# Performance work log

Hardware: AMD Instinct MI355X
Metric: run time of the kernel (lower is better)

The kernel has to match this reference:

```python
import jax, jax.numpy as jnp
import numpy as np

N, N_SPINS, N_HIDDEN = 8192, 1024, 1024


def setup_inputs() -> dict:
    key = jax.random.key(0)
    ks = jax.random.split(key, 6)
    s_in = 1.0 / np.sqrt(N_SPINS)
    s_h = 1.0 / np.sqrt(N_HIDDEN)
    return {
        "x": jax.random.normal(ks[0], (N, N_SPINS), dtype=jnp.float32),
        "W_in": jax.random.normal(ks[1], (N_HIDDEN, N_SPINS), dtype=jnp.float32) * s_in,
        "b_in": jax.random.normal(ks[2], (N_HIDDEN,), dtype=jnp.float32) * s_in,
        "Wq": jax.random.normal(ks[3], (N_HIDDEN, N_HIDDEN), dtype=jnp.float32) * s_h,
        "Wk": jax.random.normal(ks[4], (N_HIDDEN, N_HIDDEN), dtype=jnp.float32) * s_h,
        "Wv": jax.random.normal(ks[5], (N_HIDDEN, N_HIDDEN), dtype=jnp.float32) * s_h,
    }


def reference(x, W_in, b_in, Wq, Wk, Wv):
    # embedding: Linear(n_spins, n_hidden)  -> h: [N, H]
    h = x @ W_in.T + b_in
    q = h @ Wq.T                      # [N, H]
    k = h @ Wk.T                      # [N, H]
    v = h @ Wv.T                      # [N, H]
    scores = (q @ k.T) * 0.25         # [N, N], scale 1/4 as in source
    attn = jax.nn.softmax(scores, axis=0)  # softmax over dim=0 (columns)
    out = attn @ v                    # [N, H]
    # log(cosh(z)) = |z| + log1p(exp(-2|z|)) - log(2), numerically stable
    a = jnp.abs(out)
    logcosh = a + jnp.log1p(jnp.exp(-2.0 * a)) - jnp.log(jnp.asarray(2.0, out.dtype))
    return jnp.sum(logcosh, axis=-1)  # [N]
```

## Files before the change

### kernel.cpp

```cpp
#include <hip/hip_runtime.h>
#include <hip/hip_bf16.h>
#include <cstdint>
#include <cstddef>

#define NTOK 8192
#define NHID 1024

typedef __attribute__((ext_vector_type(8))) __bf16 bf16x8;
typedef __attribute__((ext_vector_type(4))) float f32x4;

__device__ __forceinline__ unsigned short f2bf(float f) {
    union { float f; unsigned u; } v; v.f = f;
    unsigned r = v.u + 0x7FFF + ((v.u >> 16) & 1);
    return (unsigned short)(r >> 16);
}

__device__ __forceinline__ float bf2f(unsigned short u) {
    union { unsigned u; float f; } v; v.u = ((unsigned)u) << 16;
    return v.f;
}

__device__ __forceinline__ void async_copy16(const void* gsrc, void* ldsdst) {
    __builtin_amdgcn_global_load_lds(
        (const __attribute__((address_space(1))) unsigned int*)gsrc,
        (__attribute__((address_space(3))) unsigned int*)ldsdst,
        16, 0, 0);
}

__device__ __forceinline__ void read_frags(
    const unsigned short* __restrict__ As, const unsigned short* __restrict__ Bs,
    int wm, int wn, int fr, int pc, bf16x8 (&a)[8], bf16x8 (&b)[4])
{
#pragma unroll
    for (int i = 0; i < 8; ++i) a[i] = *(const bf16x8*)&As[(wm + i * 16 + fr) * 64 + pc];
#pragma unroll
    for (int j = 0; j < 4; ++j) b[j] = *(const bf16x8*)&Bs[(wn + j * 16 + fr) * 64 + pc];
}

__device__ __forceinline__ void mfma32(
    const bf16x8 (&a)[8], const bf16x8 (&b)[4], f32x4 (&acc)[8][4])
{
    __builtin_amdgcn_s_setprio(1);
#pragma unroll
    for (int i = 0; i < 8; ++i)
#pragma unroll
        for (int j = 0; j < 4; ++j)
            acc[i][j] = __builtin_amdgcn_mfma_f32_16x16x32_bf16(
                a[i], b[j], acc[i][j], 0, 0, 0);
    __builtin_amdgcn_s_setprio(0);
}

template <int EPI, bool SWAP>
__global__ __launch_bounds__(512, 2) void gemm_sq2(
    const unsigned short* __restrict__ A,
    const unsigned short* __restrict__ B,
    void* __restrict__ C,
    const float* __restrict__ bias,
    float* __restrict__ zsum,
    float scale, int M, int N, int K, int lda, int ldb)
{
    __shared__ __attribute__((aligned(16))) unsigned short lds[2][32768];

    const int tid  = threadIdx.x;
    const int wave = tid >> 6;
    const int lane = tid & 63;
    const int bm = (SWAP ? blockIdx.x : blockIdx.y) * 256;
    const int bn = (SWAP ? blockIdx.y : blockIdx.x) * 256;
    const size_t ldaz = (size_t)lda;
    const size_t ldbz = (size_t)ldb;

    const int srow = lane >> 3;
    const int scol = ((lane & 7) ^ srow) * 8;
    const unsigned short* Ag[4];
    const unsigned short* Bg[4];
    int off[4];
#pragma unroll
    for (int t = 0; t < 4; ++t) {
        int r = (wave * 4 + t) * 8 + srow;
        Ag[t] = A + (size_t)(bm + r) * ldaz + scol;
        Bg[t] = B + (size_t)(bn + r) * ldbz + scol;
        off[t] = (wave * 4 + t) * 512;
    }

    const int wm = (wave >> 2) * 128;
    const int wn = (wave & 3) * 64;
    const int fr = lane & 15;
    const int frl = fr & 7;
    const int q = lane >> 4;

    const int pc0 = (q ^ frl) * 8;
    const int pc1 = ((4 + q) ^ frl) * 8;

    f32x4 acc[8][4] = {};

    const int nt = K >> 6;

    auto stageA = [&](int s) {
#pragma unroll
        for (int t = 0; t < 4; ++t) { async_copy16(Ag[t], &lds[s][off[t]]); Ag[t] += 64; }
    };
    auto stageB = [&](int s) {
#pragma unroll
        for (int t = 0; t < 4; ++t) { async_copy16(Bg[t], &lds[s][16384 + off[t]]); Bg[t] += 64; }
    };

    stageA(0);
    stageB(0);
    stageA(1);
    asm volatile("s_waitcnt vmcnt(4)" ::: "memory");
    asm volatile("s_barrier" ::: "memory");

    bf16x8 aP[8], bP[4];
    bf16x8 aQ[8], bQ[4];
    read_frags(&lds[0][0], &lds[0][16384], wm, wn, fr, pc0, aP, bP);

    for (int t = 0; t < nt; ++t) {
        const int cb = t & 1;
        const int nb = cb ^ 1;
        const unsigned short* As = &lds[cb][0];
        const unsigned short* Bs = &lds[cb][16384];

        if (t + 1 < nt) stageB(nb);
        read_frags(As, Bs, wm, wn, fr, pc1, aQ, bQ);
        __builtin_amdgcn_sched_barrier(0);
        mfma32(aP, bP, acc);
        asm volatile("s_waitcnt lgkmcnt(0)" ::: "memory");
        asm volatile("s_barrier" ::: "memory");
        if (t + 2 < nt) stageA(cb);
        if (t < nt - 2) asm volatile("s_waitcnt vmcnt(4)" ::: "memory");
        else            asm volatile("s_waitcnt vmcnt(0)" ::: "memory");
        asm volatile("s_barrier" ::: "memory");

        if (t + 1 < nt)
            read_frags(&lds[nb][0], &lds[nb][16384], wm, wn, fr, pc0, aP, bP);
        __builtin_amdgcn_sched_barrier(0);
        mfma32(aQ, bQ, acc);
    }

    const int erow = q * 4;
#pragma unroll
    for (int j = 0; j < 4; ++j) {
        const int gcol = bn + wn + j * 16 + fr;
        const float bv = (EPI == 1 && bias) ? bias[gcol] : 0.0f;
        float colsum = 0.0f;
#pragma unroll
        for (int i = 0; i < 8; ++i) {
            const int grow0 = bm + wm + i * 16 + erow;
#pragma unroll
            for (int r = 0; r < 4; ++r) {
                float v;
                if (EPI == 2) {
                    v = __expf(fmaf(acc[i][j][r], scale, -64.0f));
                    colsum += v;
                } else {
                    v = acc[i][j][r] * scale + bv;
                }
                size_t idx = (size_t)(grow0 + r) * N + gcol;
                if (EPI == 0) ((float*)C)[idx] = v;
                else          ((unsigned short*)C)[idx] = f2bf(v);
            }
        }
        if (EPI == 2) {
            colsum += __shfl_xor(colsum, 16, 64);
            colsum += __shfl_xor(colsum, 32, 64);
            if (q == 0) atomicAdd(&zsum[gcol], colsum);
        }
    }
}

template <int EPI, bool SWAP>
__global__ __launch_bounds__(512, 2) void gemm_bt4(
    const unsigned short* __restrict__ A,
    const unsigned short* __restrict__ B,
    void* __restrict__ C,
    const float* __restrict__ bias,
    float* __restrict__ zsum,
    float scale, int M, int N, int K, int lda, int ldb)
{
    __shared__ __attribute__((aligned(16))) unsigned short lds[3][24576];

    const int tid  = threadIdx.x;
    const int wave = tid >> 6;
    const int lane = tid & 63;
    const int bm = (SWAP ? blockIdx.x : blockIdx.y) * 256;
    const int bn = (SWAP ? blockIdx.y : blockIdx.x) * 128;
    const size_t ldaz = (size_t)lda;
    const size_t ldbz = (size_t)ldb;

    const int srow = lane >> 3;
    const int scol = ((lane & 7) ^ srow) * 8;
    const unsigned short* Ag[4];
    const unsigned short* Bg[2];
    int Aoff[4], Boff[2];
#pragma unroll
    for (int t = 0; t < 4; ++t) {
        int r = (wave * 4 + t) * 8 + srow;
        Ag[t] = A + (size_t)(bm + r) * ldaz + scol;
        Aoff[t] = (wave * 4 + t) * 512;
    }
#pragma unroll
    for (int t = 0; t < 2; ++t) {
        int r = (wave * 2 + t) * 8 + srow;
        Bg[t] = B + (size_t)(bn + r) * ldbz + scol;
        Boff[t] = 16384 + (wave * 2 + t) * 512;
    }

    const int wm = (wave >> 1) * 64;
    const int wn = (wave & 1) * 64;
    const int fr = lane & 15;
    const int frl = fr & 7;
    const int q = lane >> 4;

    const int pc0 = (q ^ frl) * 8;
    const int pc1 = ((4 + q) ^ frl) * 8;

    f32x4 acc[4][4] = {};

    const int nt = K >> 6;

    {
        unsigned short* b0 = &lds[0][0];
        unsigned short* b1 = &lds[1][0];
#pragma unroll
        for (int u = 0; u < 4; ++u) { async_copy16(Ag[u], b0 + Aoff[u]); Ag[u] += 64; }
#pragma unroll
        for (int u = 0; u < 2; ++u) { async_copy16(Bg[u], b0 + Boff[u]); Bg[u] += 64; }
#pragma unroll
        for (int u = 0; u < 4; ++u) { async_copy16(Ag[u], b1 + Aoff[u]); Ag[u] += 64; }
#pragma unroll
        for (int u = 0; u < 2; ++u) { async_copy16(Bg[u], b1 + Boff[u]); Bg[u] += 64; }
        asm volatile("s_waitcnt vmcnt(6)" ::: "memory");
        asm volatile("s_barrier" ::: "memory");
    }

    bf16x8 a0_0, a0_1, a0_2, a0_3, b0_0, b0_1, b0_2, b0_3;
    bf16x8 a1_0, a1_1, a1_2, a1_3, b1_0, b1_1, b1_2, b1_3;

    {
        const unsigned short* As = &lds[0][0];
        const unsigned short* Bs = &lds[0][16384];
        a0_0 = *(const bf16x8*)&As[(wm +  0 + fr) * 64 + pc0];
        a0_1 = *(const bf16x8*)&As[(wm + 16 + fr) * 64 + pc0];
        a0_2 = *(const bf16x8*)&As[(wm + 32 + fr) * 64 + pc0];
        a0_3 = *(const bf16x8*)&As[(wm + 48 + fr) * 64 + pc0];
        b0_0 = *(const bf16x8*)&Bs[(wn +  0 + fr) * 64 + pc0];
        b0_1 = *(const bf16x8*)&Bs[(wn + 16 + fr) * 64 + pc0];
        b0_2 = *(const bf16x8*)&Bs[(wn + 32 + fr) * 64 + pc0];
        b0_3 = *(const bf16x8*)&Bs[(wn + 48 + fr) * 64 + pc0];
    }

#define MFMA16(AA0, AA1, AA2, AA3, BB0, BB1, BB2, BB3)                         \
    do {                                                                       \
        __builtin_amdgcn_s_setprio(1);                                         \
        acc[0][0] = __builtin_amdgcn_mfma_f32_16x16x32_bf16(AA0, BB0, acc[0][0], 0, 0, 0); \
        acc[0][1] = __builtin_amdgcn_mfma_f32_16x16x32_bf16(AA0, BB1, acc[0][1], 0, 0, 0); \
        acc[0][2] = __builtin_amdgcn_mfma_f32_16x16x32_bf16(AA0, BB2, acc[0][2], 0, 0, 0); \
        acc[0][3] = __builtin_amdgcn_mfma_f32_16x16x32_bf16(AA0, BB3, acc[0][3], 0, 0, 0); \
        acc[1][0] = __builtin_amdgcn_mfma_f32_16x16x32_bf16(AA1, BB0, acc[1][0], 0, 0, 0); \
        acc[1][1] = __builtin_amdgcn_mfma_f32_16x16x32_bf16(AA1, BB1, acc[1][1], 0, 0, 0); \
        acc[1][2] = __builtin_amdgcn_mfma_f32_16x16x32_bf16(AA1, BB2, acc[1][2], 0, 0, 0); \
        acc[1][3] = __builtin_amdgcn_mfma_f32_16x16x32_bf16(AA1, BB3, acc[1][3], 0, 0, 0); \
        acc[2][0] = __builtin_amdgcn_mfma_f32_16x16x32_bf16(AA2, BB0, acc[2][0], 0, 0, 0); \
        acc[2][1] = __builtin_amdgcn_mfma_f32_16x16x32_bf16(AA2, BB1, acc[2][1], 0, 0, 0); \
        acc[2][2] = __builtin_amdgcn_mfma_f32_16x16x32_bf16(AA2, BB2, acc[2][2], 0, 0, 0); \
        acc[2][3] = __builtin_amdgcn_mfma_f32_16x16x32_bf16(AA2, BB3, acc[2][3], 0, 0, 0); \
        acc[3][0] = __builtin_amdgcn_mfma_f32_16x16x32_bf16(AA3, BB0, acc[3][0], 0, 0, 0); \
        acc[3][1] = __builtin_amdgcn_mfma_f32_16x16x32_bf16(AA3, BB1, acc[3][1], 0, 0, 0); \
        acc[3][2] = __builtin_amdgcn_mfma_f32_16x16x32_bf16(AA3, BB2, acc[3][2], 0, 0, 0); \
        acc[3][3] = __builtin_amdgcn_mfma_f32_16x16x32_bf16(AA3, BB3, acc[3][3], 0, 0, 0); \
        __builtin_amdgcn_s_setprio(0);                                         \
    } while (0)

    int cb = 0;
    int sb = 2;
    for (int t = 0; t < nt; ++t) {
        const bool pf = (t + 2 < nt);
        const unsigned short* As = &lds[cb][0];
        const unsigned short* Bs = &lds[cb][16384];
        unsigned short* Sb = &lds[sb][0];
        const int nb = (cb == 2) ? 0 : cb + 1;
        const unsigned short* An = &lds[nb][0];
        const unsigned short* Bn = &lds[nb][16384];

        a1_0 = *(const bf16x8*)&As[(wm +  0 + fr) * 64 + pc1];
        a1_1 = *(const bf16x8*)&As[(wm + 16 + fr) * 64 + pc1];
        a1_2 = *(const bf16x8*)&As[(wm + 32 + fr) * 64 + pc1];
        a1_3 = *(const bf16x8*)&As[(wm + 48 + fr) * 64 + pc1];
        b1_0 = *(const bf16x8*)&Bs[(wn +  0 + fr) * 64 + pc1];
        b1_1 = *(const bf16x8*)&Bs[(wn + 16 + fr) * 64 + pc1];
        b1_2 = *(const bf16x8*)&Bs[(wn + 32 + fr) * 64 + pc1];
        b1_3 = *(const bf16x8*)&Bs[(wn + 48 + fr) * 64 + pc1];
        if (pf) {
#pragma unroll
            for (int u = 0; u < 4; ++u) { async_copy16(Ag[u], Sb + Aoff[u]); Ag[u] += 64; }
        }
        __builtin_amdgcn_sched_barrier(0);
        MFMA16(a0_0, a0_1, a0_2, a0_3, b0_0, b0_1, b0_2, b0_3);
        if (t < nt - 2) asm volatile("s_waitcnt vmcnt(4)" ::: "memory");
        else            asm volatile("s_waitcnt vmcnt(0)" ::: "memory");
        asm volatile("s_barrier" ::: "memory");

        if (t + 1 < nt) {
            a0_0 = *(const bf16x8*)&An[(wm +  0 + fr) * 64 + pc0];
            a0_1 = *(const bf16x8*)&An[(wm + 16 + fr) * 64 + pc0];
            a0_2 = *(const bf16x8*)&An[(wm + 32 + fr) * 64 + pc0];
            a0_3 = *(const bf16x8*)&An[(wm + 48 + fr) * 64 + pc0];
            b0_0 = *(const bf16x8*)&Bn[(wn +  0 + fr) * 64 + pc0];
            b0_1 = *(const bf16x8*)&Bn[(wn + 16 + fr) * 64 + pc0];
            b0_2 = *(const bf16x8*)&Bn[(wn + 32 + fr) * 64 + pc0];
            b0_3 = *(const bf16x8*)&Bn[(wn + 48 + fr) * 64 + pc0];
        }
        if (pf) {
#pragma unroll
            for (int u = 0; u < 2; ++u) { async_copy16(Bg[u], Sb + Boff[u]); Bg[u] += 64; }
        }
        __builtin_amdgcn_sched_barrier(0);
        MFMA16(a1_0, a1_1, a1_2, a1_3, b1_0, b1_1, b1_2, b1_3);
        asm volatile("s_barrier" ::: "memory");

        if (pf) sb = (sb == 2) ? 0 : sb + 1;
        cb = nb;
    }
#undef MFMA16

    const int erow = q * 4;
#pragma unroll
    for (int j = 0; j < 4; ++j) {
        const int gcol = bn + wn + j * 16 + fr;
        const float bv = (EPI == 1 && bias) ? bias[gcol] : 0.0f;
        float colsum = 0.0f;
#pragma unroll
        for (int i = 0; i < 4; ++i) {
            const int grow0 = bm + wm + i * 16 + erow;
#pragma unroll
            for (int r = 0; r < 4; ++r) {
                float v;
                if (EPI == 2) {
                    v = __expf(fmaf(acc[i][j][r], scale, -64.0f));
                    colsum += v;
                } else {
                    v = acc[i][j][r] * scale + bv;
                }
                size_t idx = (size_t)(grow0 + r) * N + gcol;
                if (EPI == 0) ((float*)C)[idx] = v;
                else          ((unsigned short*)C)[idx] = f2bf(v);
            }
        }
        if (EPI == 2) {
            colsum += __shfl_xor(colsum, 16, 64);
            colsum += __shfl_xor(colsum, 32, 64);
            if (q == 0) atomicAdd(&zsum[gcol], colsum);
        }
    }
}

__global__ void cvt_all(const float4* __restrict__ x,
                        const float4* __restrict__ w0,
                        const float4* __restrict__ w1,
                        const float4* __restrict__ w2,
                        const float4* __restrict__ w3,
                        ushort4* __restrict__ xb,
                        ushort4* __restrict__ wdst,
                        float4* __restrict__ pz4,
                        int n4x, int n4w)
{
    int i = blockIdx.x * blockDim.x + threadIdx.x;
    int n4 = n4x + 4 * n4w;
    if (i >= n4) {
        int zi = i - n4;
        if (zi < 2048) pz4[zi] = make_float4(0.f, 0.f, 0.f, 0.f);
        return;
    }
    float4 f;
    ushort4* dst;
    if (i < n4x) {
        f = x[i]; dst = xb + i;
    } else {
        int r = i - n4x;
        int seg = r / n4w, off = r % n4w;
        const float4* src = (seg == 0) ? w0 : (seg == 1) ? w1 : (seg == 2) ? w2 : w3;
        f = src[off]; dst = wdst + r;
    }
    ushort4 o;
    o.x = f2bf(f.x); o.y = f2bf(f.y); o.z = f2bf(f.z); o.w = f2bf(f.w);
    *dst = o;
}

__global__ __launch_bounds__(256) void transpose_scale(
    const unsigned short* __restrict__ v,
    const float* __restrict__ z,
    unsigned short* __restrict__ vt)
{
    __shared__ float lds[64 * 65];
    const int tid = threadIdx.x;
    const int j0 = blockIdx.x * 64;
    const int h0 = blockIdx.y * 64;
    const int c = tid & 63;
    const int r0 = tid >> 6;
#pragma unroll
    for (int it = 0; it < 16; ++it) {
        int r = it * 4 + r0;
        lds[r * 65 + c] = bf2f(v[(size_t)(j0 + r) * 3072 + h0 + c]);
    }
    __syncthreads();
    const float rz = 1.0f / z[j0 + c];
#pragma unroll
    for (int it = 0; it < 16; ++it) {
        int r = it * 4 + r0;
        vt[(size_t)(h0 + r) * NTOK + j0 + c] = f2bf(lds[c * 65 + r] * rz);
    }
}

__global__ void logcosh_rowsum(const ushort4* __restrict__ O4,
                               float* __restrict__ out)
{
    const float LN2 = 0.69314718055994531f;
    int row = blockIdx.x;
    ushort4 u = O4[(size_t)row * 256 + threadIdx.x];
    float s = 0.0f, a;
    a = fabsf(bf2f(u.x)); s += a + log1pf(__expf(-2.0f * a));
    a = fabsf(bf2f(u.y)); s += a + log1pf(__expf(-2.0f * a));
    a = fabsf(bf2f(u.z)); s += a + log1pf(__expf(-2.0f * a));
    a = fabsf(bf2f(u.w)); s += a + log1pf(__expf(-2.0f * a));
    s -= 4.0f * LN2;
    for (int off = 32; off; off >>= 1) s += __shfl_down(s, off, 64);
    __shared__ float red[4];
    if ((threadIdx.x & 63) == 0) red[threadIdx.x >> 6] = s;
    __syncthreads();
    if (threadIdx.x == 0) out[row] = red[0] + red[1] + red[2] + red[3];
}

extern "C" void kernel_launch(void* const* d_in, const int* in_sizes, int n_in,
                              void* d_out, int out_size, void* d_ws, size_t ws_size,
                              hipStream_t stream)
{
    (void)in_sizes; (void)n_in; (void)out_size; (void)ws_size;

    const float* x    = (const float*)d_in[0];
    const float* W_in = (const float*)d_in[1];
    const float* b_in = (const float*)d_in[2];
    const float* Wq   = (const float*)d_in[3];
    const float* Wk   = (const float*)d_in[4];
    const float* Wv   = (const float*)d_in[5];
    float* out = (float*)d_out;

    char* w = (char*)d_ws;
    const size_t MiB = 1024 * 1024;
    unsigned short* Pb     = (unsigned short*)(w);
    unsigned short* qkv    = (unsigned short*)(w + 128 * MiB);
    unsigned short* xb     = (unsigned short*)(w + 128 * MiB);
    unsigned short* outb   = (unsigned short*)(w + 128 * MiB);
    unsigned short* hb     = (unsigned short*)(w + 176 * MiB);
    unsigned short* vtb    = (unsigned short*)(w + 176 * MiB);
    unsigned short* wib    = (unsigned short*)(w + 192 * MiB);
    unsigned short* wqkvb  = (unsigned short*)(w + 194 * MiB);
    float*          pz     = (float*)         (w + 200 * MiB);

    {
        int n4x = NTOK * NHID / 4;
        int n4w = NHID * NHID / 4;
        int n4  = n4x + 4 * n4w;
        cvt_all<<<n4 / 256 + 8, 256, 0, stream>>>(
            (const float4*)x, (const float4*)W_in, (const float4*)Wq,
            (const float4*)Wk, (const float4*)Wv,
            (ushort4*)xb, (ushort4*)wib, (float4*)pz, n4x, n4w);
    }

    dim3 gNH(NHID / 128, NTOK / 256);
    gemm_bt4<1, false><<<gNH, 512, 0, stream>>>(
        xb, wib, hb, b_in, nullptr, 1.0f, NTOK, NHID, NHID, NHID, NHID);

    dim3 gQKV(3 * NHID / 128, NTOK / 256);
    gemm_bt4<1, false><<<gQKV, 512, 0, stream>>>(
        hb, wqkvb, qkv, nullptr, nullptr, 1.0f, NTOK, 3 * NHID, NHID, NHID, NHID);

    dim3 gS(NTOK / 256, NTOK / 256);
    gemm_sq2<2, false><<<gS, 512, 0, stream>>>(
        qkv, qkv + NHID, Pb, nullptr, pz, 0.25f, NTOK, NTOK, NHID,
        3 * NHID, 3 * NHID);

    dim3 gT(NTOK / 64, NHID / 64);
    transpose_scale<<<gT, 256, 0, stream>>>(qkv + 2 * NHID, pz, vtb);

    dim3 gO(NTOK / 256, NHID / 128);
    gemm_bt4<1, true><<<gO, 512, 0, stream>>>(
        Pb, vtb, outb, nullptr, nullptr, 1.0f, NTOK, NHID, NTOK, NTOK, NTOK);

    logcosh_rowsum<<<NTOK, 256, 0, stream>>>((const ushort4*)outb, out);
}
```

Before: 487.2 us.

## Restructure score GEMM main loop into four barrier-synchronized MFMA phases

```diff
diff --git a/kernel.cpp b/kernel.cpp
--- a/kernel.cpp
+++ b/kernel.cpp
@@ -27,31 +27,8 @@
         16, 0, 0);
 }
 
-__device__ __forceinline__ void read_frags(
-    const unsigned short* __restrict__ As, const unsigned short* __restrict__ Bs,
-    int wm, int wn, int fr, int pc, bf16x8 (&a)[8], bf16x8 (&b)[4])
-{
-#pragma unroll
-    for (int i = 0; i < 8; ++i) a[i] = *(const bf16x8*)&As[(wm + i * 16 + fr) * 64 + pc];
-#pragma unroll
-    for (int j = 0; j < 4; ++j) b[j] = *(const bf16x8*)&Bs[(wn + j * 16 + fr) * 64 + pc];
-}
-
-__device__ __forceinline__ void mfma32(
-    const bf16x8 (&a)[8], const bf16x8 (&b)[4], f32x4 (&acc)[8][4])
-{
-    __builtin_amdgcn_s_setprio(1);
-#pragma unroll
-    for (int i = 0; i < 8; ++i)
-#pragma unroll
-        for (int j = 0; j < 4; ++j)
-            acc[i][j] = __builtin_amdgcn_mfma_f32_16x16x32_bf16(
-                a[i], b[j], acc[i][j], 0, 0, 0);
-    __builtin_amdgcn_s_setprio(0);
-}
-
 template <int EPI, bool SWAP>
-__global__ __launch_bounds__(512, 2) void gemm_sq2(
+__global__ __launch_bounds__(512, 2) void gemm_sq3(
     const unsigned short* __restrict__ A,
     const unsigned short* __restrict__ B,
     void* __restrict__ C,
@@ -104,66 +81,107 @@
         for (int t = 0; t < 4; ++t) { async_copy16(Bg[t], &lds[s][16384 + off[t]]); Bg[t] += 64; }
     };
 
+#define PHASE_MFMA(IBASE)                                                      \
+    do {                                                                       \
+        __builtin_amdgcn_s_setprio(1);                                         \
+        _Pragma("unroll")                                                      \
+        for (int i = 0; i < 4; ++i)                                            \
+            _Pragma("unroll")                                                  \
+            for (int j = 0; j < 4; ++j)                                        \
+                acc[(IBASE) + i][j] = __builtin_amdgcn_mfma_f32_16x16x32_bf16( \
+                    a[i], b[j], acc[(IBASE) + i][j], 0, 0, 0);                 \
+        __builtin_amdgcn_s_setprio(0);                                         \
+    } while (0)
+
     stageA(0);
     stageB(0);
-    stageA(1);
-    asm volatile("s_waitcnt vmcnt(4)" ::: "memory");
+    asm volatile("s_waitcnt vmcnt(0)" ::: "memory");
     asm volatile("s_barrier" ::: "memory");
-
-    bf16x8 aP[8], bP[4];
-    bf16x8 aQ[8], bQ[4];
-    read_frags(&lds[0][0], &lds[0][16384], wm, wn, fr, pc0, aP, bP);
 
     for (int t = 0; t < nt; ++t) {
         const int cb = t & 1;
         const int nb = cb ^ 1;
         const unsigned short* As = &lds[cb][0];
         const unsigned short* Bs = &lds[cb][16384];
-
-        if (t + 1 < nt) stageB(nb);
-        read_frags(As, Bs, wm, wn, fr, pc1, aQ, bQ);
+        const bool pf = (t + 1 < nt);
+
+        bf16x8 a[4], b[4];
+
+#pragma unroll
+        for (int i = 0; i < 4; ++i) a[i] = *(const bf16x8*)&As[(wm + i * 16 + fr) * 64 + pc0];
+#pragma unroll
+        for (int j = 0; j < 4; ++j) b[j] = *(const bf16x8*)&Bs[(wn + j * 16 + fr) * 64 + pc0];
+        if (pf) stageA(nb);
+        asm volatile("s_barrier" ::: "memory");
+        asm volatile("s_waitcnt lgkmcnt(0)" ::: "memory");
         __builtin_amdgcn_sched_barrier(0);
-        mfma32(aP, bP, acc);
+        PHASE_MFMA(0);
+        asm volatile("s_barrier" ::: "memory");
+
+#pragma unroll
+        for (int i = 0; i < 4; ++i) a[i] = *(const bf16x8*)&As[(wm + 64 + i * 16 + fr) * 64 + pc0];
+        if (pf) stageB(nb);
+        asm volatile("s_barrier" ::: "memory");
         asm volatile("s_waitcnt lgkmcnt(0)" ::: "memory");
-        asm volatile("s_barrier" ::: "memory");
-        if (t + 2 < nt) stageA(cb);
-        if (t < nt - 2) asm volatile("s_waitcnt vmcnt(4)" ::: "memory");
-        else            asm volatile("s_waitcnt vmcnt(0)" ::: "memory");
-        asm volatile("s_barrier" ::: "memory");
-
-        if (t + 1 < nt)
-            read_frags(&lds[nb][0], &lds[nb][16384], wm, wn, fr, pc0, aP, bP);
         __builtin_amdgcn_sched_barrier(0);
-        mfma32(aQ, bQ, acc);
-    }
+        PHASE_MFMA(4);
+        asm volatile("s_barrier" ::: "memory");
+
+#pragma unroll
+        for (int i = 0; i < 4; ++i) a[i] = *(const bf16x8*)&As[(wm + i * 16 + fr) * 64 + pc1];
+#pragma unroll
+        for (int j = 0; j < 4; ++j) b[j] = *(const bf16x8*)&Bs[(wn + j * 16 + fr) * 64 + pc1];
+        asm volatile("s_barrier" ::: "memory");
+        asm volatile("s_waitcnt lgkmcnt(0)" ::: "memory");
+        __builtin_amdgcn_sched_barrier(0);
+        PHASE_MFMA(0);
+        asm volatile("s_barrier" ::: "memory");
+
+#pragma unroll
+        for (int i = 0; i < 4; ++i) a[i] = *(const bf16x8*)&As[(wm + 64 + i * 16 + fr) * 64 + pc1];
+        asm volatile("s_barrier" ::: "memory");
+        asm volatile("s_waitcnt lgkmcnt(0)" ::: "memory");
+        __builtin_amdgcn_sched_barrier(0);
+        PHASE_MFMA(4);
+        if (pf) asm volatile("s_waitcnt vmcnt(0)" ::: "memory");
+        asm volatile("s_barrier" ::: "memory");
+    }
+#undef PHASE_MFMA
 
     const int erow = q * 4;
-#pragma unroll
-    for (int j = 0; j < 4; ++j) {
-        const int gcol = bn + wn + j * 16 + fr;
-        const float bv = (EPI == 1 && bias) ? bias[gcol] : 0.0f;
-        float colsum = 0.0f;
-#pragma unroll
-        for (int i = 0; i < 8; ++i) {
-            const int grow0 = bm + wm + i * 16 + erow;
-#pragma unroll
-            for (int r = 0; r < 4; ++r) {
+    float colsum[4] = {0.f, 0.f, 0.f, 0.f};
+    float bv[4];
+#pragma unroll
+    for (int j = 0; j < 4; ++j)
+        bv[j] = (EPI == 1 && bias) ? bias[bn + wn + j * 16 + fr] : 0.0f;
+#pragma unroll
+    for (int i = 0; i < 8; ++i) {
+        const int grow0 = bm + wm + i * 16 + erow;
+#pragma unroll
+        for (int r = 0; r < 4; ++r) {
+            const size_t rowoff = (size_t)(grow0 + r) * N;
+#pragma unroll
+            for (int j = 0; j < 4; ++j) {
+                const int gcol = bn + wn + j * 16 + fr;
                 float v;
                 if (EPI == 2) {
                     v = __expf(fmaf(acc[i][j][r], scale, -64.0f));
-                    colsum += v;
+                    colsum[j] += v;
                 } else {
-                    v = acc[i][j][r] * scale + bv;
+                    v = acc[i][j][r] * scale + bv[j];
                 }
-                size_t idx = (size_t)(grow0 + r) * N + gcol;
-                if (EPI == 0) ((float*)C)[idx] = v;
-                else          ((unsigned short*)C)[idx] = f2bf(v);
+                if (EPI == 0) ((float*)C)[rowoff + gcol] = v;
+                else          ((unsigned short*)C)[rowoff + gcol] = f2bf(v);
             }
         }
-        if (EPI == 2) {
-            colsum += __shfl_xor(colsum, 16, 64);
-            colsum += __shfl_xor(colsum, 32, 64);
-            if (q == 0) atomicAdd(&zsum[gcol], colsum);
+    }
+    if (EPI == 2) {
+#pragma unroll
+        for (int j = 0; j < 4; ++j) {
+            float cs = colsum[j];
+            cs += __shfl_xor(cs, 16, 64);
+            cs += __shfl_xor(cs, 32, 64);
+            if (q == 0) atomicAdd(&zsum[bn + wn + j * 16 + fr], cs);
         }
     }
 }
@@ -475,7 +493,7 @@
         hb, wqkvb, qkv, nullptr, nullptr, 1.0f, NTOK, 3 * NHID, NHID, NHID, NHID);
 
     dim3 gS(NTOK / 256, NTOK / 256);
-    gemm_sq2<2, false><<<gS, 512, 0, stream>>>(
+    gemm_sq3<2, false><<<gS, 512, 0, stream>>>(
         qkv, qkv + NHID, Pb, nullptr, pz, 0.25f, NTOK, NTOK, NHID,
         3 * NHID, 3 * NHID);
 
```

Measured after the change: 452.0 us. -7.2%, faster.
